# Kernel optimization log

Hardware: AMD Instinct MI355X
Metric: run time of the kernel (lower is better)

The kernel has to match this reference:

```python
import jax, jax.numpy as jnp
import numpy as np

B, N, DH = 256, 32, 128      # batch, n_agents, per-agent hidden
E = 496                       # n_edges (fully connected over 32 agents)
DIM_IN = 2 * DH               # 256, MLP input (concat of two agent states)
DIM_HID = 256
A = 12                        # dim_act
R = 4                         # payoff_rank
DIM_OUT = 2 * R * A           # 96


def setup_inputs() -> dict:
    key = jax.random.key(0)
    ks = jax.random.split(key, 7)
    hidden_states_n = jax.random.normal(ks[0], (B, N, DH), dtype=jnp.float32)
    edges_from = jax.random.randint(ks[1], (E,), 0, N, dtype=jnp.int32).astype(jnp.int64)
    edges_to = jax.random.randint(ks[2], (E,), 0, N, dtype=jnp.int32).astype(jnp.int64)
    # torch.nn.Linear params: W [out, in], b [out]
    W1 = jax.random.normal(ks[3], (DIM_HID, DIM_IN), dtype=jnp.float32) * (1.0 / np.sqrt(DIM_IN))
    b1 = jnp.zeros((DIM_HID,), dtype=jnp.float32)
    W2 = jax.random.normal(ks[4], (DIM_OUT, DIM_HID), dtype=jnp.float32) * (1.0 / np.sqrt(DIM_HID))
    b2 = jnp.zeros((DIM_OUT,), dtype=jnp.float32)
    return {"hidden_states_n": hidden_states_n, "W1": W1, "b1": b1, "W2": W2,
            "b2": b2, "edges_from": edges_from, "edges_to": edges_to}


def reference(hidden_states_n, W1, b1, W2, b2, edges_from, edges_to):
    hf = hidden_states_n[:, edges_from]                     # [B, E, DH]
    ht = hidden_states_n[:, edges_to]                       # [B, E, DH]
    # stack of (from||to, to||from): [2, B, E, 2*DH]
    inp = jnp.stack([jnp.concatenate([hf, ht], axis=-1),
                     jnp.concatenate([ht, hf], axis=-1)], axis=0)
    h = jax.nn.relu(inp @ W1.T + b1)                        # [2, B, E, DIM_HID]
    p = h @ W2.T + b2                                       # [2, B, E, 2*R*A]
    p = p.reshape(2, B, E, R, 2, A)
    # low-rank outer product per rank, summed over ranks: [2, B, E, A, A]
    payoffs = jnp.einsum('sberi,sberj->sbeij', p[..., 0, :], p[..., 1, :])
    # second copy is transposed, then mean over the two directions
    return 0.5 * (payoffs[0] + jnp.swapaxes(payoffs[1], -1, -2))  # [B, E, A, A]
```

## Files before the change

kernel.cpp:

```cpp
#include <hip/hip_runtime.h>

typedef unsigned int uint;
typedef _Float16 f16;

typedef __attribute__((ext_vector_type(8))) _Float16 f16x8;
typedef __attribute__((ext_vector_type(2))) _Float16 f16x2;
typedef __attribute__((ext_vector_type(4))) float f32x4;

#define E_CNT 496

#define W2_STRIDE 264
#define W2_STAGE_BYTES 52224
#define W2_CHUNKS 51
#define LDS_BYTES 52224

#define PP_STRIDE 136
#define V_OFF 1088
#define PW_F16 2176

#define XS_STRIDE 264
#define XH_BYTES 33792

__device__ __forceinline__ uint pack2_f16(float lo, float hi) {
    union { f16x2 h; uint u; } r;
    r.h[0] = (_Float16)lo;
    r.h[1] = (_Float16)hi;
    return r.u;
}

__device__ __forceinline__ void load_lds16(const void* g, void* l) {
    __builtin_amdgcn_global_load_lds(
        (const __attribute__((address_space(1))) void*)g,
        (__attribute__((address_space(3))) void*)l, 16, 0, 0);
}

__global__ __launch_bounds__(256) void x_kernel(
    const float* __restrict__ hidden, const float* __restrict__ W1,
    const float* __restrict__ b1, f16* __restrict__ Xout,
    const float* __restrict__ W2, f16* __restrict__ w2h) {
    __shared__ __align__(16) unsigned char xsmem[XH_BYTES + 64 * XS_STRIDE * 2];
    float* hs = (float*)xsmem;
    f16* xs = (f16*)(xsmem + XH_BYTES);

    const int tid = threadIdx.x;

    if (blockIdx.x == 256) {
        #pragma unroll
        for (int j = 0; j < 24; ++j) {
            int idx4 = tid + j * 256;
            int n = idx4 >> 6;
            int k = (idx4 & 63) << 2;
            float4 v = *(const float4*)&W2[n * 256 + k];
            uint2 o;
            o.x = pack2_f16(v.x, v.y);
            o.y = pack2_f16(v.z, v.w);
            *(uint2*)&w2h[n * W2_STRIDE + k] = o;
        }
        return;
    }

    const int rowblock = blockIdx.x >> 1;
    const int half = blockIdx.x & 1;
    const int ln = tid & 63;
    const int waveId = tid >> 6;
    const int quad = ln >> 4;
    const int l16 = ln & 15;
    const int row0 = rowblock * 64;

    {
        const float* src = hidden + row0 * 128;
        #pragma unroll
        for (int it = 0; it < 8; ++it) {
            int idx = it * 256 + tid;
            int r = idx >> 5;
            int c4 = idx & 31;
            float4 v = *(const float4*)(src + idx * 4);
            *(float4*)&hs[r * 132 + c4 * 4] = v;
        }
    }
    __syncthreads();

    union FU { uint u[4]; f16x8 v; };

    #pragma unroll
    for (int p = 0; p < 2; ++p) {
        FU wf[2][4];
        float bh[2][4];
        #pragma unroll
        for (int nt = 0; nt < 2; ++nt) {
            const int tl = p * 8 + waveId * 2 + nt;
            const float* wrow = W1 + (tl * 16 + l16) * 256 + half * 128 + quad * 8;
            #pragma unroll
            for (int kk = 0; kk < 4; ++kk) {
                float4 v0 = *(const float4*)(wrow + kk * 32);
                float4 v1 = *(const float4*)(wrow + kk * 32 + 4);
                wf[nt][kk].u[0] = pack2_f16(v0.x, v0.y);
                wf[nt][kk].u[1] = pack2_f16(v0.z, v0.w);
                wf[nt][kk].u[2] = pack2_f16(v1.x, v1.y);
                wf[nt][kk].u[3] = pack2_f16(v1.z, v1.w);
            }
            #pragma unroll
            for (int r = 0; r < 4; ++r)
                bh[nt][r] = 0.5f * b1[tl * 16 + quad * 4 + r];
        }

        #pragma unroll
        for (int ch = 0; ch < 4; ++ch) {
            FU hf[4];
            const float* hrow = &hs[(ch * 16 + l16) * 132 + quad * 8];
            #pragma unroll
            for (int kk = 0; kk < 4; ++kk) {
                float4 v0 = *(const float4*)(hrow + kk * 32);
                float4 v1 = *(const float4*)(hrow + kk * 32 + 4);
                hf[kk].u[0] = pack2_f16(v0.x, v0.y);
                hf[kk].u[1] = pack2_f16(v0.z, v0.w);
                hf[kk].u[2] = pack2_f16(v1.x, v1.y);
                hf[kk].u[3] = pack2_f16(v1.z, v1.w);
            }
            #pragma unroll
            for (int nt = 0; nt < 2; ++nt) {
                const int tl = p * 8 + waveId * 2 + nt;
                f32x4 acc = (f32x4){0.f, 0.f, 0.f, 0.f};
                #pragma unroll
                for (int kk = 0; kk < 4; ++kk)
                    acc = __builtin_amdgcn_mfma_f32_16x16x32_f16(wf[nt][kk].v, hf[kk].v, acc, 0, 0, 0);
                uint2 o;
                o.x = pack2_f16(acc[0] + bh[nt][0], acc[1] + bh[nt][1]);
                o.y = pack2_f16(acc[2] + bh[nt][2], acc[3] + bh[nt][3]);
                *(uint2*)&xs[(ch * 16 + l16) * XS_STRIDE + tl * 16 + quad * 4] = o;
            }
        }
    }

    __syncthreads();

    f16* xdst = Xout + half * (8192 * 256) + row0 * 256;
    #pragma unroll
    for (int it = 0; it < 8; ++it) {
        int idx = it * 256 + tid;
        int row = idx >> 5;
        int c8 = idx & 31;
        uint4 v = *(const uint4*)&xs[row * XS_STRIDE + c8 * 8];
        *(uint4*)&xdst[row * 256 + c8 * 8] = v;
    }
}

__global__ __launch_bounds__(512, 6) void gemm_payoff_kernel(
    const f16* __restrict__ X1, const f16* __restrict__ X2,
    const int* __restrict__ e_f, const int* __restrict__ e_t,
    const f16* __restrict__ w2g, const float* __restrict__ b2,
    float* __restrict__ out) {

    __shared__ __align__(16) unsigned char smem[LDS_BYTES];
    f16* w2s = (f16*)smem;

    const int tid = threadIdx.x;
    const int ln = tid & 63;
    const int waveId = tid >> 6;
    const int quad = ln >> 4;
    const int l16 = ln & 15;
    const int pl = l16 & 7;
    const int s = l16 >> 3;

    const int bx = blockIdx.x;
    const int lb = (bx & 7) * 248 + (bx >> 3);

    {
        const unsigned char* src = (const unsigned char*)w2g + ln * 16;
        #pragma unroll
        for (int j = 0; j < 7; ++j) {
            int i = waveId + j * 8;
            if (i < W2_CHUNKS)
                load_lds16(src + i * 1024, smem + i * 1024);
        }
    }

    bool f64 = true, t64 = true;
    #pragma unroll
    for (int i = 0; i < 16; ++i) {
        if (e_f[2 * i + 1] != 0) f64 = false;
        if (e_t[2 * i + 1] != 0) t64 = false;
    }

    const int pairBase = lb * 64 + waveId * 8;
    const f16* px1;
    const f16* px2;
    {
        int pair = pairBase + pl;
        int b = pair / E_CNT;
        int e = pair - b * E_CNT;
        int f = f64 ? e_f[2 * e] : e_f[e];
        int t = t64 ? e_t[2 * e] : e_t[e];
        int n1 = s ? t : f;
        int n2 = s ? f : t;
        px1 = X1 + ((b * 32 + n1) * 256 + quad * 8);
        px2 = X2 + ((b * 32 + n2) * 256 + quad * 8);
    }

    f32x4 acc[6];
    #pragma unroll
    for (int tt = 0; tt < 6; ++tt) acc[tt] = (f32x4){0.f, 0.f, 0.f, 0.f};

    typedef union { uint4 q; f16x8 h; } XU;
    XU G1[4], G2[4];
    #pragma unroll
    for (int c = 0; c < 4; ++c) {
        G1[c].q = *(const uint4*)(px1 + c * 32);
        G2[c].q = *(const uint4*)(px2 + c * 32);
    }

    const f16x8 zero8 = (f16x8){0, 0, 0, 0, 0, 0, 0, 0};

    __syncthreads();

    #pragma unroll
    for (int kk = 0; kk < 8; ++kk) {
        const int buf = kk & 3;
        f16x8 sum = G1[buf].h + G2[buf].h;
        f16x8 af = __builtin_elementwise_max(sum, zero8);
        if (kk < 4) {
            G1[buf].q = *(const uint4*)(px1 + (kk + 4) * 32);
            G2[buf].q = *(const uint4*)(px2 + (kk + 4) * 32);
        }
        #pragma unroll
        for (int tt = 0; tt < 6; ++tt) {
            f16x8 bf = *(const f16x8*)&w2s[(tt * 16 + l16) * W2_STRIDE + kk * 32 + quad * 8];
            acc[tt] = __builtin_amdgcn_mfma_f32_16x16x32_f16(af, bf, acc[tt], 0, 0, 0);
        }
    }

    float b2v[6];
    #pragma unroll
    for (int tt = 0; tt < 6; ++tt) b2v[tt] = b2[tt * 16 + l16];

    int d6[6];
    float psc[6];
    {
        const int s_ = quad >> 1;
        #pragma unroll
        for (int tt = 0; tt < 6; ++tt) {
            int n = tt * 16 + l16;
            int rr = n / 24;
            int rem = n - rr * 24;
            int c01 = (rem >= 12) ? 1 : 0;
            int a = rem - c01 * 12;
            int k8 = s_ * 4 + rr;
            int toL = (c01 == s_) ? 1 : 0;
            d6[tt] = (toL ? 0 : V_OFF) + (quad & 1) * 4 * PP_STRIDE + a * 8 + k8;
            psc[tt] = toL ? 0.5f : 1.0f;
        }
    }

    __syncthreads();

    f16* pm = (f16*)smem + waveId * PW_F16;

    #pragma unroll
    for (int tt = 0; tt < 6; ++tt) {
        #pragma unroll
        for (int r = 0; r < 4; ++r)
            pm[d6[tt] + r * PP_STRIDE] = (_Float16)((acc[tt][r] + b2v[tt]) * psc[tt]);
    }

    #pragma unroll
    for (int pp = 0; pp < 8; ++pp) {
        f16x8 afp = zero8, bfp = zero8;
        if (quad == 0) {
            afp = *(const f16x8*)&pm[V_OFF + pp * PP_STRIDE + l16 * 8];
            bfp = *(const f16x8*)&pm[pp * PP_STRIDE + l16 * 8];
        }
        f32x4 d = __builtin_amdgcn_mfma_f32_16x16x32_f16(
            afp, bfp, (f32x4){0.f, 0.f, 0.f, 0.f}, 0, 0, 0);
        if (l16 < 12 && quad < 3) {
            float* ob = out + (pairBase + pp) * 144 + l16 * 12 + quad * 4;
            *(float4*)ob = make_float4(d[0], d[1], d[2], d[3]);
        }
    }
}

extern "C" void kernel_launch(void* const* d_in, const int* in_sizes, int n_in,
                              void* d_out, int out_size, void* d_ws, size_t ws_size,
                              hipStream_t stream) {
    const float* hidden = (const float*)d_in[0];
    const float* W1 = (const float*)d_in[1];
    const float* b1 = (const float*)d_in[2];
    const float* W2 = (const float*)d_in[3];
    const float* b2 = (const float*)d_in[4];
    const int* e_f = (const int*)d_in[5];
    const int* e_t = (const int*)d_in[6];
    float* out = (float*)d_out;

    char* ws = (char*)d_ws;
    f16* X = (f16*)ws;
    f16* w2h = (f16*)(ws + 8 * 1024 * 1024);

    x_kernel<<<257, 256, 0, stream>>>(hidden, W1, b1, X, W2, w2h);
    gemm_payoff_kernel<<<1984, 512, 0, stream>>>(X, X + 8192 * 256, e_f, e_t, w2h, b2, out);
}
```

Measured before the change: 130.7 us.

## Split output tiles across wave pairs, each wave handling two pair-groups

Each pair of waves now shares two 8-pair groups, with each wave computing three of the six output column tiles for both groups, so every W2 fragment read from LDS feeds two MFMAs. This halves per-wave W2 LDS traffic and accumulator count but duplicates the gather of X rows across the two waves of a pair and shortens the prefetch depth from four to two chunks. An extra barrier is added because partner waves now write into each other's payoff staging region before the outer-product stage.

Result: slower. 155.9 us (+19.3%).

```diff
diff --git a/kernel.cpp b/kernel.cpp
--- a/kernel.cpp
+++ b/kernel.cpp
@@ -161,6 +161,7 @@
     const int l16 = ln & 15;
     const int pl = l16 & 7;
     const int s = l16 >> 3;
+    const int ttBase = (waveId & 1) * 3;
 
     const int bx = blockIdx.x;
     const int lb = (bx & 7) * 248 + (bx >> 3);
@@ -182,31 +183,36 @@
         if (e_t[2 * i + 1] != 0) t64 = false;
     }
 
-    const int pairBase = lb * 64 + waveId * 8;
-    const f16* px1;
-    const f16* px2;
-    {
-        int pair = pairBase + pl;
+    const int pairGrp = lb * 64 + (waveId & 6) * 8;
+    const f16* px1[2];
+    const f16* px2[2];
+    #pragma unroll
+    for (int g = 0; g < 2; ++g) {
+        int pair = pairGrp + g * 8 + pl;
         int b = pair / E_CNT;
         int e = pair - b * E_CNT;
         int f = f64 ? e_f[2 * e] : e_f[e];
         int t = t64 ? e_t[2 * e] : e_t[e];
         int n1 = s ? t : f;
         int n2 = s ? f : t;
-        px1 = X1 + ((b * 32 + n1) * 256 + quad * 8);
-        px2 = X2 + ((b * 32 + n2) * 256 + quad * 8);
-    }
-
-    f32x4 acc[6];
-    #pragma unroll
-    for (int tt = 0; tt < 6; ++tt) acc[tt] = (f32x4){0.f, 0.f, 0.f, 0.f};
+        px1[g] = X1 + ((b * 32 + n1) * 256 + quad * 8);
+        px2[g] = X2 + ((b * 32 + n2) * 256 + quad * 8);
+    }
+
+    f32x4 acc[2][3];
+    #pragma unroll
+    for (int g = 0; g < 2; ++g)
+        #pragma unroll
+        for (int t3 = 0; t3 < 3; ++t3) acc[g][t3] = (f32x4){0.f, 0.f, 0.f, 0.f};
 
     typedef union { uint4 q; f16x8 h; } XU;
-    XU G1[4], G2[4];
-    #pragma unroll
-    for (int c = 0; c < 4; ++c) {
-        G1[c].q = *(const uint4*)(px1 + c * 32);
-        G2[c].q = *(const uint4*)(px2 + c * 32);
+    XU G1[2][2], G2[2][2];
+    #pragma unroll
+    for (int g = 0; g < 2; ++g) {
+        G1[0][g].q = *(const uint4*)(px1[g] + 0 * 32);
+        G2[0][g].q = *(const uint4*)(px2[g] + 0 * 32);
+        G1[1][g].q = *(const uint4*)(px1[g] + 1 * 32);
+        G2[1][g].q = *(const uint4*)(px2[g] + 1 * 32);
     }
 
     const f16x8 zero8 = (f16x8){0, 0, 0, 0, 0, 0, 0, 0};
@@ -215,53 +221,65 @@
 
     #pragma unroll
     for (int kk = 0; kk < 8; ++kk) {
-        const int buf = kk & 3;
-        f16x8 sum = G1[buf].h + G2[buf].h;
-        f16x8 af = __builtin_elementwise_max(sum, zero8);
-        if (kk < 4) {
-            G1[buf].q = *(const uint4*)(px1 + (kk + 4) * 32);
-            G2[buf].q = *(const uint4*)(px2 + (kk + 4) * 32);
-        }
-        #pragma unroll
-        for (int tt = 0; tt < 6; ++tt) {
-            f16x8 bf = *(const f16x8*)&w2s[(tt * 16 + l16) * W2_STRIDE + kk * 32 + quad * 8];
-            acc[tt] = __builtin_amdgcn_mfma_f32_16x16x32_f16(af, bf, acc[tt], 0, 0, 0);
-        }
-    }
-
-    float b2v[6];
-    #pragma unroll
-    for (int tt = 0; tt < 6; ++tt) b2v[tt] = b2[tt * 16 + l16];
-
-    int d6[6];
-    float psc[6];
+        const int buf = kk & 1;
+        f16x8 af[2];
+        #pragma unroll
+        for (int g = 0; g < 2; ++g) {
+            f16x8 sum = G1[buf][g].h + G2[buf][g].h;
+            af[g] = __builtin_elementwise_max(sum, zero8);
+        }
+        if (kk < 6) {
+            #pragma unroll
+            for (int g = 0; g < 2; ++g) {
+                G1[buf][g].q = *(const uint4*)(px1[g] + (kk + 2) * 32);
+                G2[buf][g].q = *(const uint4*)(px2[g] + (kk + 2) * 32);
+            }
+        }
+        #pragma unroll
+        for (int t3 = 0; t3 < 3; ++t3) {
+            f16x8 bf = *(const f16x8*)&w2s[((ttBase + t3) * 16 + l16) * W2_STRIDE + kk * 32 + quad * 8];
+            acc[0][t3] = __builtin_amdgcn_mfma_f32_16x16x32_f16(af[0], bf, acc[0][t3], 0, 0, 0);
+            acc[1][t3] = __builtin_amdgcn_mfma_f32_16x16x32_f16(af[1], bf, acc[1][t3], 0, 0, 0);
+        }
+    }
+
+    float b2v[3];
+    int d6[3];
+    float psc[3];
     {
         const int s_ = quad >> 1;
         #pragma unroll
-        for (int tt = 0; tt < 6; ++tt) {
-            int n = tt * 16 + l16;
+        for (int t3 = 0; t3 < 3; ++t3) {
+            int n = (ttBase + t3) * 16 + l16;
+            b2v[t3] = b2[n];
             int rr = n / 24;
             int rem = n - rr * 24;
             int c01 = (rem >= 12) ? 1 : 0;
             int a = rem - c01 * 12;
             int k8 = s_ * 4 + rr;
             int toL = (c01 == s_) ? 1 : 0;
-            d6[tt] = (toL ? 0 : V_OFF) + (quad & 1) * 4 * PP_STRIDE + a * 8 + k8;
-            psc[tt] = toL ? 0.5f : 1.0f;
+            d6[t3] = (toL ? 0 : V_OFF) + (quad & 1) * 4 * PP_STRIDE + a * 8 + k8;
+            psc[t3] = toL ? 0.5f : 1.0f;
+        }
+    }
+
+    __syncthreads();
+
+    #pragma unroll
+    for (int g = 0; g < 2; ++g) {
+        f16* pmg = (f16*)smem + ((waveId & 6) + g) * PW_F16;
+        #pragma unroll
+        for (int t3 = 0; t3 < 3; ++t3) {
+            #pragma unroll
+            for (int r = 0; r < 4; ++r)
+                pmg[d6[t3] + r * PP_STRIDE] = (_Float16)((acc[g][t3][r] + b2v[t3]) * psc[t3]);
         }
     }
 
     __syncthreads();
 
     f16* pm = (f16*)smem + waveId * PW_F16;
-
-    #pragma unroll
-    for (int tt = 0; tt < 6; ++tt) {
-        #pragma unroll
-        for (int r = 0; r < 4; ++r)
-            pm[d6[tt] + r * PP_STRIDE] = (_Float16)((acc[tt][r] + b2v[tt]) * psc[tt]);
-    }
-
+    const int pairBase = lb * 64 + waveId * 8;
     #pragma unroll
     for (int pp = 0; pp < 8; ++pp) {
         f16x8 afp = zero8, bfp = zero8;
```

## Make gemm_payoff blocks persistent over eight pair groups to amortize W2 LDS load

Applied to the files above, without the earlier changes.

The GEMM+payoff kernel now launches 248 blocks instead of 1984. Each block loops over 8 groups of 64 edge pairs, so the 52KB W2 staging into LDS is paid once per block rather than once per 64 pairs. The next group's X gathers are issued before the payoff epilogue to overlap global loads with output work. Per-wave payoff scratch moves to its own LDS region so W2 stays resident, which raises LDS per block to about 87KB. Occupancy hint drops to 2 blocks per CU, and 248 blocks on the device means fewer waves in flight to hide latency.

New measurement: 130.8 us. Within noise of the previous version (+0.1%).

```diff
diff --git a/kernel.cpp b/kernel.cpp
--- a/kernel.cpp
+++ b/kernel.cpp
@@ -10,13 +10,13 @@
 #define E_CNT 496
 
 #define W2_STRIDE 264
-#define W2_STAGE_BYTES 52224
 #define W2_CHUNKS 51
-#define LDS_BYTES 52224
+#define W2_LDS 52224
 
 #define PP_STRIDE 136
 #define V_OFF 1088
 #define PW_F16 2176
+#define GEMM_LDS (W2_LDS + 8 * 4352)
 
 #define XS_STRIDE 264
 #define XH_BYTES 33792
@@ -145,14 +145,15 @@
     }
 }
 
-__global__ __launch_bounds__(512, 6) void gemm_payoff_kernel(
+__global__ __launch_bounds__(512, 2) void gemm_payoff_kernel(
     const f16* __restrict__ X1, const f16* __restrict__ X2,
     const int* __restrict__ e_f, const int* __restrict__ e_t,
     const f16* __restrict__ w2g, const float* __restrict__ b2,
     float* __restrict__ out) {
 
-    __shared__ __align__(16) unsigned char smem[LDS_BYTES];
+    __shared__ __align__(16) unsigned char smem[GEMM_LDS];
     f16* w2s = (f16*)smem;
+    f16* pmBase = (f16*)(smem + W2_LDS);
 
     const int tid = threadIdx.x;
     const int ln = tid & 63;
@@ -163,7 +164,7 @@
     const int s = l16 >> 3;
 
     const int bx = blockIdx.x;
-    const int lb = (bx & 7) * 248 + (bx >> 3);
+    const int lb = (bx & 7) * 31 + (bx >> 3);
 
     {
         const unsigned char* src = (const unsigned char*)w2g + ln * 16;
@@ -182,57 +183,7 @@
         if (e_t[2 * i + 1] != 0) t64 = false;
     }
 
-    const int pairBase = lb * 64 + waveId * 8;
-    const f16* px1;
-    const f16* px2;
-    {
-        int pair = pairBase + pl;
-        int b = pair / E_CNT;
-        int e = pair - b * E_CNT;
-        int f = f64 ? e_f[2 * e] : e_f[e];
-        int t = t64 ? e_t[2 * e] : e_t[e];
-        int n1 = s ? t : f;
-        int n2 = s ? f : t;
-        px1 = X1 + ((b * 32 + n1) * 256 + quad * 8);
-        px2 = X2 + ((b * 32 + n2) * 256 + quad * 8);
-    }
-
-    f32x4 acc[6];
-    #pragma unroll
-    for (int tt = 0; tt < 6; ++tt) acc[tt] = (f32x4){0.f, 0.f, 0.f, 0.f};
-
-    typedef union { uint4 q; f16x8 h; } XU;
-    XU G1[4], G2[4];
-    #pragma unroll
-    for (int c = 0; c < 4; ++c) {
-        G1[c].q = *(const uint4*)(px1 + c * 32);
-        G2[c].q = *(const uint4*)(px2 + c * 32);
-    }
-
-    const f16x8 zero8 = (f16x8){0, 0, 0, 0, 0, 0, 0, 0};
-
-    __syncthreads();
-
-    #pragma unroll
-    for (int kk = 0; kk < 8; ++kk) {
-        const int buf = kk & 3;
-        f16x8 sum = G1[buf].h + G2[buf].h;
-        f16x8 af = __builtin_elementwise_max(sum, zero8);
-        if (kk < 4) {
-            G1[buf].q = *(const uint4*)(px1 + (kk + 4) * 32);
-            G2[buf].q = *(const uint4*)(px2 + (kk + 4) * 32);
-        }
-        #pragma unroll
-        for (int tt = 0; tt < 6; ++tt) {
-            f16x8 bf = *(const f16x8*)&w2s[(tt * 16 + l16) * W2_STRIDE + kk * 32 + quad * 8];
-            acc[tt] = __builtin_amdgcn_mfma_f32_16x16x32_f16(af, bf, acc[tt], 0, 0, 0);
-        }
-    }
-
     float b2v[6];
-    #pragma unroll
-    for (int tt = 0; tt < 6; ++tt) b2v[tt] = b2[tt * 16 + l16];
-
     int d6[6];
     float psc[6];
     {
@@ -240,6 +191,7 @@
         #pragma unroll
         for (int tt = 0; tt < 6; ++tt) {
             int n = tt * 16 + l16;
+            b2v[tt] = b2[n];
             int rr = n / 24;
             int rem = n - rr * 24;
             int c01 = (rem >= 12) ? 1 : 0;
@@ -251,29 +203,89 @@
         }
     }
 
+    auto computePx = [&](int g, const f16*& p1, const f16*& p2) {
+        int pair = lb * 512 + g * 64 + waveId * 8 + pl;
+        int b = pair / E_CNT;
+        int e = pair - b * E_CNT;
+        int f = f64 ? e_f[2 * e] : e_f[e];
+        int t = t64 ? e_t[2 * e] : e_t[e];
+        int n1 = s ? t : f;
+        int n2 = s ? f : t;
+        p1 = X1 + ((b * 32 + n1) * 256 + quad * 8);
+        p2 = X2 + ((b * 32 + n2) * 256 + quad * 8);
+    };
+
+    typedef union { uint4 q; f16x8 h; } XU;
+    XU G1[4], G2[4];
+    const f16* px1;
+    const f16* px2;
+
+    computePx(0, px1, px2);
+    #pragma unroll
+    for (int c = 0; c < 4; ++c) {
+        G1[c].q = *(const uint4*)(px1 + c * 32);
+        G2[c].q = *(const uint4*)(px2 + c * 32);
+    }
+
+    const f16x8 zero8 = (f16x8){0, 0, 0, 0, 0, 0, 0, 0};
+    f16* pm = pmBase + waveId * PW_F16;
+
     __syncthreads();
 
-    f16* pm = (f16*)smem + waveId * PW_F16;
-
-    #pragma unroll
-    for (int tt = 0; tt < 6; ++tt) {
-        #pragma unroll
-        for (int r = 0; r < 4; ++r)
-            pm[d6[tt] + r * PP_STRIDE] = (_Float16)((acc[tt][r] + b2v[tt]) * psc[tt]);
-    }
-
-    #pragma unroll
-    for (int pp = 0; pp < 8; ++pp) {
-        f16x8 afp = zero8, bfp = zero8;
-        if (quad == 0) {
-            afp = *(const f16x8*)&pm[V_OFF + pp * PP_STRIDE + l16 * 8];
-            bfp = *(const f16x8*)&pm[pp * PP_STRIDE + l16 * 8];
-        }
-        f32x4 d = __builtin_amdgcn_mfma_f32_16x16x32_f16(
-            afp, bfp, (f32x4){0.f, 0.f, 0.f, 0.f}, 0, 0, 0);
-        if (l16 < 12 && quad < 3) {
-            float* ob = out + (pairBase + pp) * 144 + l16 * 12 + quad * 4;
-            *(float4*)ob = make_float4(d[0], d[1], d[2], d[3]);
+    f32x4 acc[6];
+
+    #pragma unroll 1
+    for (int g = 0; g < 8; ++g) {
+        #pragma unroll
+        for (int tt = 0; tt < 6; ++tt) acc[tt] = (f32x4){0.f, 0.f, 0.f, 0.f};
+
+        #pragma unroll
+        for (int kk = 0; kk < 8; ++kk) {
+            const int buf = kk & 3;
+            f16x8 sum = G1[buf].h + G2[buf].h;
+            f16x8 af = __builtin_elementwise_max(sum, zero8);
+            if (kk < 4) {
+                G1[buf].q = *(const uint4*)(px1 + (kk + 4) * 32);
+                G2[buf].q = *(const uint4*)(px2 + (kk + 4) * 32);
+            }
+            #pragma unroll
+            for (int tt = 0; tt < 6; ++tt) {
+                f16x8 bf = *(const f16x8*)&w2s[(tt * 16 + l16) * W2_STRIDE + kk * 32 + quad * 8];
+                acc[tt] = __builtin_amdgcn_mfma_f32_16x16x32_f16(af, bf, acc[tt], 0, 0, 0);
+            }
+        }
+
+        const int pairBase = lb * 512 + g * 64 + waveId * 8;
+
+        if (g < 7) {
+            computePx(g + 1, px1, px2);
+            #pragma unroll
+            for (int c = 0; c < 4; ++c) {
+                G1[c].q = *(const uint4*)(px1 + c * 32);
+                G2[c].q = *(const uint4*)(px2 + c * 32);
+            }
+        }
+
+        #pragma unroll
+        for (int tt = 0; tt < 6; ++tt) {
+            #pragma unroll
+            for (int r = 0; r < 4; ++r)
+                pm[d6[tt] + r * PP_STRIDE] = (_Float16)((acc[tt][r] + b2v[tt]) * psc[tt]);
+        }
+
+        #pragma unroll
+        for (int pp = 0; pp < 8; ++pp) {
+            f16x8 afp = zero8, bfp = zero8;
+            if (quad == 0) {
+                afp = *(const f16x8*)&pm[V_OFF + pp * PP_STRIDE + l16 * 8];
+                bfp = *(const f16x8*)&pm[pp * PP_STRIDE + l16 * 8];
+            }
+            f32x4 d = __builtin_amdgcn_mfma_f32_16x16x32_f16(
+                afp, bfp, (f32x4){0.f, 0.f, 0.f, 0.f}, 0, 0, 0);
+            if (l16 < 12 && quad < 3) {
+                float* ob = out + (pairBase + pp) * 144 + l16 * 12 + quad * 4;
+                *(float4*)ob = make_float4(d[0], d[1], d[2], d[3]);
+            }
         }
     }
 }
@@ -295,5 +307,5 @@
     f16* w2h = (f16*)(ws + 8 * 1024 * 1024);
 
     x_kernel<<<257, 256, 0, stream>>>(hidden, W1, b1, X, W2, w2h);
-    gemm_payoff_kernel<<<1984, 512, 0, stream>>>(X, X + 8192 * 256, e_f, e_t, w2h, b2, out);
-}
+    gemm_payoff_kernel<<<248, 512, 0, stream>>>(X, X + 8192 * 256, e_f, e_t, w2h, b2, out);
+}
```
